# Performance work log

Measured on AMD Instinct MI355X. Metric: run time of the kernel, lower is better.

The kernel has to match this reference:

```python
import jax, jax.numpy as jnp
import numpy as np

DEPTH = 4
HEADS = 8
DIM_HEAD = 32
NUM_CLUSTERS = 64
KMEANS_ITERS = 10
EPS = 1e-5


def layer_norm(x, g, b):
    m = jnp.mean(x, axis=-1, keepdims=True)
    v = jnp.var(x, axis=-1, keepdims=True)
    return (x - m) * jax.lax.rsqrt(v + EPS) * g + b


def kmeans_cluster(xf, k, iters):
    # xf: [P, D]. Lloyd's algorithm with deterministic init (first k points).
    centers = xf[:k]
    x_sq = jnp.sum(xf * xf, axis=-1, keepdims=True)  # [P,1]

    def assign(c):
        # squared distances [P, K]
        d = x_sq - 2.0 * (xf @ c.T) + jnp.sum(c * c, axis=-1)[None, :]
        return jnp.argmin(d, axis=-1)

    def step(c, _):
        labels = assign(c)
        sums = jax.ops.segment_sum(xf, labels, num_segments=k)
        counts = jax.ops.segment_sum(jnp.ones((xf.shape[0],), xf.dtype), labels, num_segments=k)
        new_c = jnp.where(counts[:, None] > 0, sums / jnp.maximum(counts, 1.0)[:, None], c)
        return new_c, None

    centers, _ = jax.lax.scan(step, centers, None, length=iters)
    labels = assign(centers)
    return centers[labels]  # gather: [P, D]


def setup_inputs() -> dict:
    key = jax.random.key(0)
    ks = jax.random.split(key, 8)
    B, N, D, L, M = 8, 1024, 256, DEPTH, 1024
    s = 0.02
    return {
        "x": jax.random.normal(ks[0], (B, N, D), jnp.float32),
        "ln1_g": jnp.ones((L, D), jnp.float32),
        "ln1_b": jnp.zeros((L, D), jnp.float32),
        "Wq": jax.random.normal(ks[1], (L, D, HEADS * DIM_HEAD), jnp.float32) * s,
        "Wkv": jax.random.normal(ks[2], (L, D, 2 * HEADS * DIM_HEAD), jnp.float32) * s,
        "Wo": jax.random.normal(ks[3], (L, HEADS * DIM_HEAD, D), jnp.float32) * s,
        "bo": jnp.zeros((L, D), jnp.float32),
        "ln2_g": jnp.ones((L, D), jnp.float32),
        "ln2_b": jnp.zeros((L, D), jnp.float32),
        "W1": jax.random.normal(ks[4], (L, D, M), jnp.float32) * s,
        "b1": jnp.zeros((L, M), jnp.float32),
        "W2": jax.random.normal(ks[5], (L, M, D), jnp.float32) * s,
        "b2": jnp.zeros((L, D), jnp.float32),
        "kW": jax.random.normal(ks[6], (D, D), jnp.float32) * s,
        "kb": jnp.zeros((D,), jnp.float32),
    }


def reference(x, ln1_g, ln1_b, Wq, Wkv, Wo, bo, ln2_g, ln2_b, W1, b1, W2, b2, kW, kb):
    B, N, D = x.shape
    h, dh = HEADS, DIM_HEAD
    scale = dh ** -0.5
    for l in range(DEPTH):
        # PreNorm self-attention + residual
        xn = layer_norm(x, ln1_g[l], ln1_b[l])
        q = (xn @ Wq[l]).reshape(B, N, h, dh)
        kv = xn @ Wkv[l]
        k, v = jnp.split(kv, 2, axis=-1)
        k = k.reshape(B, N, h, dh)
        v = v.reshape(B, N, h, dh)
        dots = jnp.einsum("bqhd,bkhd->bhqk", q, k) * scale
        attn = jax.nn.softmax(dots, axis=-1)
        out = jnp.einsum("bhqk,bkhd->bqhd", attn, v).reshape(B, N, h * dh)
        x = out @ Wo[l] + bo[l] + x
        # PreNorm FFN + residual
        xn = layer_norm(x, ln2_g[l], ln2_b[l])
        hdd = jax.nn.gelu(xn @ W1[l] + b1[l], approximate=False)
        x = hdd @ W2[l] + b2[l] + x
    # KMeans module: cluster flattened tokens, gather centers, linear transform.
    xf = x.reshape(B * N, D)
    clustered = kmeans_cluster(xf, NUM_CLUSTERS, KMEANS_ITERS)
    clustered = jax.lax.stop_gradient(clustered)  # torch detaches before sklearn
    clustered = clustered.reshape(B, N, D)
    return clustered @ kW + kb
```

## Files before the change

kernel.cpp:

```cpp
#include <hip/hip_runtime.h>
#include <hip/hip_bf16.h>
#include <math.h>

#define BN 8192
#define DMODEL 256
#define FFN 1024
#define NCLUST 64

typedef unsigned short u16;
typedef unsigned int u32;
typedef __attribute__((ext_vector_type(8))) short s16x8;
typedef __attribute__((ext_vector_type(8))) unsigned short u16x8;
typedef __attribute__((ext_vector_type(4))) unsigned short u16x4;
typedef __attribute__((ext_vector_type(4))) float f32x4;

__device__ __forceinline__ float bf2f(u16 v) {
    union { unsigned int u; float f; } w; w.u = ((unsigned int)v) << 16; return w.f;
}
__device__ __forceinline__ u16 f2bf(float f) {
    union { float f; unsigned int u; } w; w.f = f;
    unsigned int r = w.u + 0x7fffu + ((w.u >> 16) & 1u);
    return (u16)(r >> 16);
}
__device__ __forceinline__ u32 cvtpk(float lo, float hi) {
    u32 r;
    asm("v_cvt_pk_bf16_f32 %0, %1, %2" : "=v"(r) : "v"(lo), "v"(hi));
    return r;
}
__device__ __forceinline__ float u2f(u32 u) { union { u32 u; float f; } w; w.u = u; return w.f; }

__device__ __forceinline__ void gl16(const u16* g, u16* l) {
    __builtin_amdgcn_global_load_lds((const __attribute__((address_space(1))) u32*)g,
                                     (__attribute__((address_space(3))) u32*)l, 16, 0, 0);
}

#define BARRIER_LGKM() asm volatile("s_waitcnt lgkmcnt(0)\n\ts_barrier" ::: "memory")
#define MEMFENCE_ORDER() asm volatile("" ::: "memory")

__device__ __forceinline__ int sw32(int row, int col) { return row * 32 + (col ^ (((row >> 1) & 3) << 3)); }
__device__ __forceinline__ int sw64(int row, int col) { return row * 64 + (col ^ ((row & 7) << 3)); }
template<int BK>
__device__ __forceinline__ int swk(int row, int col) {
    if constexpr (BK == 32) return row * 32 + (col ^ (((row >> 1) & 3) << 3));
    else                    return row * 64 + (col ^ ((row & 7) << 3));
}

__global__ __launch_bounds__(256) void ln_wave(const float* __restrict__ x, const float* __restrict__ g,
                                               const float* __restrict__ b, u16* __restrict__ yh,
                                               u16* __restrict__ yl) {
    int t = threadIdx.x, w = t >> 6, l = t & 63;
    int row = blockIdx.x * 4 + w;
    const float* xr = x + (size_t)row * DMODEL;
    float4 v = *reinterpret_cast<const float4*>(xr + l * 4);
    float s = v.x + v.y + v.z + v.w;
    for (int off = 1; off < 64; off <<= 1) s += __shfl_xor(s, off);
    float mean = s * (1.0f / 256.0f);
    float4 dv = make_float4(v.x - mean, v.y - mean, v.z - mean, v.w - mean);
    float vs = dv.x * dv.x + dv.y * dv.y + dv.z * dv.z + dv.w * dv.w;
    for (int off = 1; off < 64; off <<= 1) vs += __shfl_xor(vs, off);
    float rs = rsqrtf(vs * (1.0f / 256.0f) + 1e-5f);
    float4 gg = *reinterpret_cast<const float4*>(g + l * 4);
    float4 bb = *reinterpret_cast<const float4*>(b + l * 4);
    float os[4] = {dv.x * rs * gg.x + bb.x, dv.y * rs * gg.y + bb.y,
                   dv.z * rs * gg.z + bb.z, dv.w * rs * gg.w + bb.w};
    u16x4 hv, lv;
#pragma unroll
    for (int j = 0; j < 4; j++) { u16 hh = f2bf(os[j]); hv[j] = hh; lv[j] = f2bf(os[j] - bf2f(hh)); }
    size_t o = (size_t)row * DMODEL + l * 4;
    *reinterpret_cast<u16x4*>(yh + o) = hv;
    *reinterpret_cast<u16x4*>(yl + o) = lv;
}

__device__ __forceinline__ void wconv_body(const float* __restrict__ W, u16* __restrict__ th,
                                           u16* __restrict__ tl, int K, int N, int bx, int by) {
    __shared__ float T[64][65];
    int k0 = by * 64, n0 = bx * 64;
    int t = threadIdx.x;
    int r = t >> 4, c4 = (t & 15) * 4;
#pragma unroll
    for (int i = 0; i < 4; i++) {
        float4 x = *reinterpret_cast<const float4*>(W + (size_t)(k0 + r + 16 * i) * N + n0 + c4);
        T[r + 16 * i][c4] = x.x; T[r + 16 * i][c4 + 1] = x.y;
        T[r + 16 * i][c4 + 2] = x.z; T[r + 16 * i][c4 + 3] = x.w;
    }
    __syncthreads();
#pragma unroll
    for (int i = 0; i < 4; i++) {
        int n = r + 16 * i;
        u16x4 h4, l4;
#pragma unroll
        for (int j = 0; j < 4; j++) {
            float v = T[c4 + j][n];
            u16 h = f2bf(v);
            h4[j] = h; l4[j] = f2bf(v - bf2f(h));
        }
        *reinterpret_cast<u16x4*>(th + (size_t)(n0 + n) * K + k0 + c4) = h4;
        *reinterpret_cast<u16x4*>(tl + (size_t)(n0 + n) * K + k0 + c4) = l4;
    }
}

__global__ __launch_bounds__(256) void wconv_all(const float* __restrict__ Wq, const float* __restrict__ Wkv,
                                                 const float* __restrict__ Wo, const float* __restrict__ W1,
                                                 const float* __restrict__ W2,
                                                 u16* __restrict__ wqkvh, u16* __restrict__ wqkvl,
                                                 u16* __restrict__ woh, u16* __restrict__ wol,
                                                 u16* __restrict__ w1h, u16* __restrict__ w1l,
                                                 u16* __restrict__ w2h, u16* __restrict__ w2l) {
    int f = blockIdx.x;
    if (f < 16)       wconv_body(Wq,  wqkvh,               wqkvl,               256, 256,  f & 3,  f >> 2);
    else if (f < 48)  { int g = f - 16;  wconv_body(Wkv, wqkvh + 65536,       wqkvl + 65536,       256, 512,  g & 7,  g >> 3); }
    else if (f < 64)  { int g = f - 48;  wconv_body(Wo,  woh,                 wol,                 256, 256,  g & 3,  g >> 2); }
    else if (f < 128) { int g = f - 64;  wconv_body(W1,  w1h,                 w1l,                 256, 1024, g & 15, g >> 4); }
    else              { int g = f - 128; wconv_body(W2,  w2h,                 w2l,                 1024, 256, g & 3,  g >> 2); }
}

template<int BM, int BNT, int BK>
__global__ __launch_bounds__(256) void gemm_t(const u16* __restrict__ Ath, const u16* __restrict__ Atl,
                                              const u16* __restrict__ Bth, const u16* __restrict__ Btl,
                                              const float* __restrict__ bias, const float* __restrict__ resid,
                                              float* __restrict__ Cf, u16* __restrict__ Ch, u16* __restrict__ Cl,
                                              int M, int N, int K, int fuse_gelu) {
    __shared__ u16 Ah[2][BM * BK], Al[2][BM * BK];
    __shared__ u16 Bh[2][BNT * BK], Bl[2][BNT * BK];
    constexpr int WAVES_N = (BM == 128 && BNT == 64) ? 1 : 2;
    constexpr int WAVES_M = 4 / WAVES_N;
    constexpr int MI = BM / (16 * WAVES_M);
    constexpr int NI = BNT / (16 * WAVES_N);
    constexpr int SEGS = (BM + BNT) * BK / 1024;
    constexpr int ROWS_SEG = 512 / BK;
    constexpr int ASEG = BM / ROWS_SEG;
    constexpr int BSEG = BNT / ROWS_SEG;
    int t = threadIdx.x;
    int m0 = blockIdx.y * BM, n0 = blockIdx.x * BNT;
    int L = t & 63, w = t >> 6, fr = L & 15, quad = L >> 4;
    int wm = (WAVES_N == 1) ? w : (w & 1);
    int wn = (WAVES_N == 1) ? 0 : (w >> 1);

    const u16* gsrc[SEGS];
    u16* ldst[SEGS];
    u32 dlt[SEGS];
    {
        int lr, lc;
        if constexpr (BK == 32) { lr = L >> 2; lc = (L & 3) * 8; }
        else                    { lr = L >> 3; lc = (L & 7) * 8; }
#pragma unroll
        for (int i = 0; i < SEGS; i++) {
            int s = w * SEGS + i;
            const u16* gb; u16* lb; int r; u32 d;
            if (s < ASEG)                 { gb = Ath + (size_t)m0 * K; lb = &Ah[0][0]; r = s * ROWS_SEG;                 d = BM * BK; }
            else if (s < 2 * ASEG)        { gb = Atl + (size_t)m0 * K; lb = &Al[0][0]; r = (s - ASEG) * ROWS_SEG;        d = BM * BK; }
            else if (s < 2 * ASEG + BSEG) { gb = Bth + (size_t)n0 * K; lb = &Bh[0][0]; r = (s - 2 * ASEG) * ROWS_SEG;    d = BNT * BK; }
            else                          { gb = Btl + (size_t)n0 * K; lb = &Bl[0][0]; r = (s - 2 * ASEG - BSEG) * ROWS_SEG; d = BNT * BK; }
            int row = r + lr;
            int scol;
            if constexpr (BK == 32) scol = lc ^ (((row >> 1) & 3) << 3);
            else                    scol = lc ^ ((row & 7) << 3);
            gsrc[i] = gb + (size_t)row * K + scol;
            ldst[i] = lb + r * BK;
            dlt[i] = d;
        }
    }

    f32x4 acc[MI][NI];
#pragma unroll
    for (int i = 0; i < MI; i++)
#pragma unroll
        for (int j = 0; j < NI; j++) acc[i][j] = (f32x4){0.0f, 0.0f, 0.0f, 0.0f};

    const int NT = K / BK;
#pragma unroll
    for (int i = 0; i < SEGS; i++) gl16(gsrc[i], ldst[i]);

    for (int tt = 0; tt < NT; tt++) {
        asm volatile("s_waitcnt lgkmcnt(0)" ::: "memory");
        __builtin_amdgcn_s_barrier();
        if (tt + 1 < NT) {
            int k0n = (tt + 1) * BK;
            u32 sel = (u32)((tt + 1) & 1);
#pragma unroll
            for (int i = 0; i < SEGS; i++) gl16(gsrc[i] + k0n, ldst[i] + sel * dlt[i]);
            asm volatile("s_waitcnt vmcnt(%0)" :: "n"(SEGS) : "memory");
        } else {
            asm volatile("s_waitcnt vmcnt(0)" ::: "memory");
        }
        __builtin_amdgcn_s_barrier();
        __builtin_amdgcn_sched_barrier(0);
        int cb = tt & 1;
        const u16* AhB = &Ah[cb][0]; const u16* AlB = &Al[cb][0];
        const u16* BhB = &Bh[cb][0]; const u16* BlB = &Bl[cb][0];
#pragma unroll
        for (int kk = 0; kk < BK / 32; kk++) {
            int kc = kk * 32 + quad * 8;
            s16x8 ah[MI], al[MI];
#pragma unroll
            for (int mi = 0; mi < MI; mi++) {
                int row = wm * (MI * 16) + mi * 16 + fr;
                ah[mi] = *reinterpret_cast<const s16x8*>(&AhB[swk<BK>(row, kc)]);
                al[mi] = *reinterpret_cast<const s16x8*>(&AlB[swk<BK>(row, kc)]);
            }
            __builtin_amdgcn_s_setprio(1);
#pragma unroll
            for (int ni = 0; ni < NI; ni++) {
                int rn = wn * (NI * 16) + ni * 16 + fr;
                s16x8 bhf = *reinterpret_cast<const s16x8*>(&BhB[swk<BK>(rn, kc)]);
                s16x8 blf = *reinterpret_cast<const s16x8*>(&BlB[swk<BK>(rn, kc)]);
#pragma unroll
                for (int mi = 0; mi < MI; mi++) {
                    acc[mi][ni] = __builtin_amdgcn_mfma_f32_16x16x32_bf16(ah[mi], bhf, acc[mi][ni], 0, 0, 0);
                    acc[mi][ni] = __builtin_amdgcn_mfma_f32_16x16x32_bf16(ah[mi], blf, acc[mi][ni], 0, 0, 0);
                    acc[mi][ni] = __builtin_amdgcn_mfma_f32_16x16x32_bf16(al[mi], bhf, acc[mi][ni], 0, 0, 0);
                }
            }
            __builtin_amdgcn_s_setprio(0);
        }
    }
#pragma unroll
    for (int mi = 0; mi < MI; mi++) {
#pragma unroll
        for (int ni = 0; ni < NI; ni++) {
#pragma unroll
            for (int r = 0; r < 4; r++) {
                int row = m0 + wm * (MI * 16) + mi * 16 + quad * 4 + r;
                int col = n0 + wn * (NI * 16) + ni * 16 + fr;
                float v = acc[mi][ni][r];
                if (bias) v += bias[col];
                if (fuse_gelu) v = 0.5f * v * (1.0f + erff(v * 0.70710678118654752f));
                if (resid) v += resid[(size_t)row * N + col];
                size_t o = (size_t)row * N + col;
                if (Cf) Cf[o] = v;
                if (Ch) { u16 hh = f2bf(v); Ch[o] = hh; Cl[o] = f2bf(v - bf2f(hh)); }
            }
        }
    }
}

__global__ __launch_bounds__(256) void attn14(const u16* __restrict__ qkvh, const u16* __restrict__ qkvl,
                                              u16* __restrict__ aoh, u16* __restrict__ aol) {
    int bh = blockIdx.x, b = bh >> 3, h = bh & 7;
    int qt = blockIdx.y;
    int t = threadIdx.x, L = t & 63, w = t >> 6;
    int fr = L & 15, quad = L >> 4;
    __shared__ u16 KH[2][64 * 32], KL[2][64 * 32];
    __shared__ u16 VTH[32 * 64], VTL[32 * 64];
    __shared__ u16 PH[4][16 * 64], PL[4][16 * 64];
    const float scale = 0.17677669529663687f;
    const int ROWS = 768;

    const u16* ksrc[2];
    u16* kdst[2];
    {
        int lr = L >> 2, lc = (L & 3) * 8;
#pragma unroll
        for (int i = 0; i < 2; i++) {
            int s = w * 2 + i;
            const u16* gb = (s < 4) ? qkvh : qkvl;
            u16* lb = (s < 4) ? &KH[0][0] : &KL[0][0];
            int r = (s & 3) * 16;
            int row = r + lr;
            int scol = lc ^ (((row >> 1) & 3) << 3);
            ksrc[i] = gb + ((size_t)(b * 1024) + row) * ROWS + 256 + h * 32 + scol;
            kdst[i] = lb + r * 32;
        }
    }

    size_t qoff0 = (size_t)(b * 1024 + qt * 128 + w * 16 + fr) * ROWS + h * 32 + quad * 8;
    s16x8 aqh0 = *reinterpret_cast<const s16x8*>(qkvh + qoff0);
    s16x8 aql0 = *reinterpret_cast<const s16x8*>(qkvl + qoff0);
    s16x8 aqh1 = *reinterpret_cast<const s16x8*>(qkvh + qoff0 + (size_t)64 * ROWS);
    s16x8 aql1 = *reinterpret_cast<const s16x8*>(qkvl + qoff0 + (size_t)64 * ROWS);

    int vp = t >> 3, vd0 = (t & 7) * 4;
    const u16* vh_ptr = qkvh + (size_t)(b * 1024 + 2 * vp) * ROWS + 512 + h * 32 + vd0;
    const u16* vl_ptr = qkvl + (size_t)(b * 1024 + 2 * vp) * ROWS + 512 + h * 32 + vd0;
    u16x4 vh0, vh1, vl0, vl1;
#define LOADV(kt_) do { size_t o_ = (size_t)((kt_) * 64) * ROWS;                                  \
        vh0 = *reinterpret_cast<const u16x4*>(vh_ptr + o_);                                       \
        vh1 = *reinterpret_cast<const u16x4*>(vh_ptr + o_ + ROWS);                                \
        vl0 = *reinterpret_cast<const u16x4*>(vl_ptr + o_);                                       \
        vl1 = *reinterpret_cast<const u16x4*>(vl_ptr + o_ + ROWS); } while (0)

    gl16(ksrc[0], kdst[0]);
    gl16(ksrc[1], kdst[1]);
    MEMFENCE_ORDER();
    LOADV(0);

    float m_0 = -1e30f, l_0 = 0.0f, m_1 = -1e30f, l_1 = 0.0f;
    f32x4 accA0, accA1, accB0, accB1;
    accA0 = (f32x4){0.0f, 0.0f, 0.0f, 0.0f}; accA1 = accA0; accB0 = accA0; accB1 = accA0;

#define SM_PV(SV, M_I, L_I, ACC0, ACC1) do {                                                      \
        float p[16];                                                                              \
        float ml = -1e30f;                                                                        \
        _Pragma("unroll")                                                                         \
        for (int ni = 0; ni < 4; ni++)                                                            \
            _Pragma("unroll")                                                                     \
            for (int r = 0; r < 4; r++) { float v = SV[ni][r] * scale; p[ni * 4 + r] = v; ml = fmaxf(ml, v); } \
        ml = fmaxf(ml, __shfl_xor(ml, 16));                                                       \
        ml = fmaxf(ml, __shfl_xor(ml, 32));                                                       \
        float mnew = fmaxf(M_I, ml);                                                              \
        float alpha = __expf(M_I - mnew);                                                         \
        M_I = mnew;                                                                               \
        float rs = 0.0f;                                                                          \
        _Pragma("unroll")                                                                         \
        for (int i = 0; i < 16; i++) { float e = __expf(p[i] - mnew); p[i] = e; rs += e; }        \
        rs += __shfl_xor(rs, 16);                                                                 \
        rs += __shfl_xor(rs, 32);                                                                 \
        L_I = L_I * alpha + rs;                                                                   \
        _Pragma("unroll")                                                                         \
        for (int ni = 0; ni < 4; ni++) {                                                          \
            float p0 = p[ni * 4], p1 = p[ni * 4 + 1], p2 = p[ni * 4 + 2], p3 = p[ni * 4 + 3];     \
            u32 qh01 = cvtpk(p0, p1), qh23 = cvtpk(p2, p3);                                       \
            float e0 = p0 - u2f(qh01 << 16);                                                      \
            float e1 = p1 - u2f(qh01 & 0xffff0000u);                                              \
            float e2 = p2 - u2f(qh23 << 16);                                                      \
            float e3 = p3 - u2f(qh23 & 0xffff0000u);                                              \
            u32 ql01 = cvtpk(e0, e1), ql23 = cvtpk(e2, e3);                                       \
            int c0 = sw64(fr, ni * 16 + quad * 4);                                                \
            int c1 = sw64(fr, ni * 16 + quad * 4 + 2);                                            \
            *reinterpret_cast<u32*>(&PH[w][c0]) = qh01;                                           \
            *reinterpret_cast<u32*>(&PH[w][c1]) = qh23;                                           \
            *reinterpret_cast<u32*>(&PL[w][c0]) = ql01;                                           \
            *reinterpret_cast<u32*>(&PL[w][c1]) = ql23;                                           \
        }                                                                                         \
        float a4[4];                                                                              \
        _Pragma("unroll")                                                                         \
        for (int r = 0; r < 4; r++) a4[r] = __shfl(alpha, quad * 4 + r);                          \
        ACC0[0] *= a4[0]; ACC0[1] *= a4[1]; ACC0[2] *= a4[2]; ACC0[3] *= a4[3];                   \
        ACC1[0] *= a4[0]; ACC1[1] *= a4[1]; ACC1[2] *= a4[2]; ACC1[3] *= a4[3];                   \
        __builtin_amdgcn_s_setprio(1);                                                            \
        _Pragma("unroll")                                                                         \
        for (int ks = 0; ks < 2; ks++) {                                                          \
            s16x8 aph = *reinterpret_cast<s16x8*>(&PH[w][sw64(fr, ks * 32 + quad * 8)]);          \
            s16x8 apl = *reinterpret_cast<s16x8*>(&PL[w][sw64(fr, ks * 32 + quad * 8)]);          \
            s16x8 bvh0 = *reinterpret_cast<s16x8*>(&VTH[sw64(fr, ks * 32 + quad * 8)]);           \
            s16x8 bvl0 = *reinterpret_cast<s16x8*>(&VTL[sw64(fr, ks * 32 + quad * 8)]);           \
            ACC0 = __builtin_amdgcn_mfma_f32_16x16x32_bf16(aph, bvh0, ACC0, 0, 0, 0);             \
            ACC0 = __builtin_amdgcn_mfma_f32_16x16x32_bf16(aph, bvl0, ACC0, 0, 0, 0);             \
            ACC0 = __builtin_amdgcn_mfma_f32_16x16x32_bf16(apl, bvh0, ACC0, 0, 0, 0);             \
            s16x8 bvh1 = *reinterpret_cast<s16x8*>(&VTH[sw64(16 + fr, ks * 32 + quad * 8)]);      \
            s16x8 bvl1 = *reinterpret_cast<s16x8*>(&VTL[sw64(16 + fr, ks * 32 + quad * 8)]);      \
            ACC1 = __builtin_amdgcn_mfma_f32_16x16x32_bf16(aph, bvh1, ACC1, 0, 0, 0);             \
            ACC1 = __builtin_amdgcn_mfma_f32_16x16x32_bf16(aph, bvl1, ACC1, 0, 0, 0);             \
            ACC1 = __builtin_amdgcn_mfma_f32_16x16x32_bf16(apl, bvh1, ACC1, 0, 0, 0);             \
        }                                                                                         \
        __builtin_amdgcn_s_setprio(0);                                                            \
    } while (0)

#pragma unroll 2
    for (int kt = 0; kt < 16; kt++) {
        int cur = kt & 1;
        BARRIER_LGKM();
        if (kt < 15) {
            size_t koff = (size_t)((kt + 1) * 64) * ROWS;
            u32 sel = (u32)((kt + 1) & 1) * (64 * 32);
            gl16(ksrc[0] + koff, kdst[0] + sel);
            gl16(ksrc[1] + koff, kdst[1] + sel);
        }
        {
#pragma unroll
            for (int i = 0; i < 4; i++) {
                int idx = sw64(vd0 + i, 2 * vp);
                *reinterpret_cast<u32*>(&VTH[idx]) = (u32)vh0[i] | ((u32)vh1[i] << 16);
                *reinterpret_cast<u32*>(&VTL[idx]) = (u32)vl0[i] | ((u32)vl1[i] << 16);
            }
        }
        BARRIER_LGKM();
        f32x4 sv0[4], sv1[4];
        __builtin_amdgcn_s_setprio(1);
#pragma unroll
        for (int ni = 0; ni < 4; ni++) {
            s16x8 bkh = *reinterpret_cast<s16x8*>(&KH[cur][sw32(ni * 16 + fr, quad * 8)]);
            s16x8 bkl = *reinterpret_cast<s16x8*>(&KL[cur][sw32(ni * 16 + fr, quad * 8)]);
            f32x4 c0 = (f32x4){0.0f, 0.0f, 0.0f, 0.0f};
            c0 = __builtin_amdgcn_mfma_f32_16x16x32_bf16(bkh, aqh0, c0, 0, 0, 0);
            c0 = __builtin_amdgcn_mfma_f32_16x16x32_bf16(bkl, aqh0, c0, 0, 0, 0);
            c0 = __builtin_amdgcn_mfma_f32_16x16x32_bf16(bkh, aql0, c0, 0, 0, 0);
            sv0[ni] = c0;
            f32x4 c1 = (f32x4){0.0f, 0.0f, 0.0f, 0.0f};
            c1 = __builtin_amdgcn_mfma_f32_16x16x32_bf16(bkh, aqh1, c1, 0, 0, 0);
            c1 = __builtin_amdgcn_mfma_f32_16x16x32_bf16(bkl, aqh1, c1, 0, 0, 0);
            c1 = __builtin_amdgcn_mfma_f32_16x16x32_bf16(bkh, aql1, c1, 0, 0, 0);
            sv1[ni] = c1;
        }
        __builtin_amdgcn_s_setprio(0);
        if (kt < 15) LOADV(kt + 1);
        SM_PV(sv0, m_0, l_0, accA0, accA1);
        SM_PV(sv1, m_1, l_1, accB0, accB1);
    }
#undef SM_PV
#undef LOADV
    float invl0 = 1.0f / l_0, invl1 = 1.0f / l_1;
#pragma unroll
    for (int r = 0; r < 4; r++) {
        float iv0 = __shfl(invl0, quad * 4 + r);
        float iv1 = __shfl(invl1, quad * 4 + r);
        size_t rb0 = ((size_t)(b * 1024 + qt * 128 + w * 16 + quad * 4 + r)) * DMODEL + h * 32;
        size_t rb1 = rb0 + (size_t)64 * DMODEL;
        float v0 = accA0[r] * iv0, v1 = accA1[r] * iv0;
        u16 h0 = f2bf(v0); aoh[rb0 + fr] = h0;      aol[rb0 + fr] = f2bf(v0 - bf2f(h0));
        u16 h1 = f2bf(v1); aoh[rb0 + 16 + fr] = h1; aol[rb0 + 16 + fr] = f2bf(v1 - bf2f(h1));
        float v2 = accB0[r] * iv1, v3 = accB1[r] * iv1;
        u16 h2 = f2bf(v2); aoh[rb1 + fr] = h2;      aol[rb1 + fr] = f2bf(v2 - bf2f(h2));
        u16 h3 = f2bf(v3); aoh[rb1 + 16 + fr] = h3; aol[rb1 + 16 + fr] = f2bf(v3 - bf2f(h3));
    }
}

__global__ __launch_bounds__(64) void csq_k(const float* __restrict__ centers, float* __restrict__ csq) {
    int j = blockIdx.x, l = threadIdx.x;
    float4 c4 = *reinterpret_cast<const float4*>(centers + j * DMODEL + l * 4);
    float s = c4.x * c4.x + c4.y * c4.y + c4.z * c4.z + c4.w * c4.w;
    for (int off = 1; off < 64; off <<= 1) s += __shfl_xor(s, off);
    if (l == 0) csq[j] = s;
}

__global__ __launch_bounds__(256) void km_distmin(const float* __restrict__ A, const float* __restrict__ Cn,
                                                  const float* __restrict__ csq, int* __restrict__ labels) {
    __shared__ float As[16][34];
    __shared__ float Bs[16][64];
    int t = threadIdx.x, tx = t & 15, ty = t >> 4;
    int m0 = blockIdx.x * 32;
    int mr = t & 31, kq = (t >> 5) * 2;
    int jb = t & 63, kb = (t >> 6) * 4;
    float acc[2][4] = {};
    for (int k0 = 0; k0 < 256; k0 += 16) {
        __syncthreads();
        {
            float2 a2 = *reinterpret_cast<const float2*>(A + (size_t)(m0 + mr) * DMODEL + k0 + kq);
            As[kq][mr] = a2.x; As[kq + 1][mr] = a2.y;
        }
        {
            float4 c4 = *reinterpret_cast<const float4*>(Cn + (size_t)jb * DMODEL + k0 + kb);
            Bs[kb][jb] = c4.x; Bs[kb + 1][jb] = c4.y; Bs[kb + 2][jb] = c4.z; Bs[kb + 3][jb] = c4.w;
        }
        __syncthreads();
#pragma unroll
        for (int kk = 0; kk < 16; kk++) {
            float2 a2v = *reinterpret_cast<float2*>(&As[kk][ty * 2]);
            float4 b4 = *reinterpret_cast<float4*>(&Bs[kk][tx * 4]);
            float a[2] = {a2v.x, a2v.y};
            float bf[4] = {b4.x, b4.y, b4.z, b4.w};
#pragma unroll
            for (int i = 0; i < 2; i++)
#pragma unroll
                for (int j = 0; j < 4; j++) acc[i][j] += a[i] * bf[j];
        }
    }
    float4 cs4 = *reinterpret_cast<const float4*>(csq + tx * 4);
    float csv[4] = {cs4.x, cs4.y, cs4.z, cs4.w};
#pragma unroll
    for (int i = 0; i < 2; i++) {
        float best = csv[0] - 2.0f * acc[i][0]; int bi = tx * 4;
#pragma unroll
        for (int j = 1; j < 4; j++) {
            float v = csv[j] - 2.0f * acc[i][j];
            if (v < best) { best = v; bi = tx * 4 + j; }
        }
        for (int off = 1; off < 16; off <<= 1) {
            float ov = __shfl_xor(best, off);
            int oi = __shfl_xor(bi, off);
            if (ov < best || (ov == best && oi < bi)) { best = ov; bi = oi; }
        }
        if (tx == 0) labels[m0 + ty * 2 + i] = bi;
    }
}

__global__ __launch_bounds__(256) void km_segsum(const int* __restrict__ labels, const float* __restrict__ xf,
                                                 float* __restrict__ sums16, float* __restrict__ counts16) {
    int c = blockIdx.x, j = blockIdx.y, t = threadIdx.x;
    __shared__ int labs[512];
    if (t < 128) {
        int4 l4 = *reinterpret_cast<const int4*>(labels + c * 512 + t * 4);
        labs[t * 4] = l4.x; labs[t * 4 + 1] = l4.y; labs[t * 4 + 2] = l4.z; labs[t * 4 + 3] = l4.w;
    }
    __syncthreads();
    float acc = 0.0f, cnt = 0.0f;
    const float* xb = xf + (size_t)c * 512 * DMODEL;
    for (int i = 0; i < 512; i++) {
        if (labs[i] == j) { acc += xb[(size_t)i * DMODEL + t]; cnt += 1.0f; }
    }
    sums16[((size_t)c * NCLUST + j) * DMODEL + t] = acc;
    if (t == 0) counts16[c * NCLUST + j] = cnt;
}

__global__ __launch_bounds__(256) void km_update(float* __restrict__ centers, const float* __restrict__ sums16,
                                                 const float* __restrict__ counts16, float* __restrict__ csq) {
    __shared__ float red[256];
    int j = blockIdx.x, d = threadIdx.x;
    float c = 0.0f;
#pragma unroll
    for (int cc = 0; cc < 16; cc++) c += counts16[cc * NCLUST + j];
    float sv = 0.0f;
#pragma unroll
    for (int cc = 0; cc < 16; cc++) sv += sums16[((size_t)cc * NCLUST + j) * DMODEL + d];
    float cv = centers[j * DMODEL + d];
    if (c > 0.0f) cv = sv / fmaxf(c, 1.0f);
    centers[j * DMODEL + d] = cv;
    red[d] = cv * cv;
    __syncthreads();
    for (int off = 128; off; off >>= 1) { if (d < off) red[d] += red[d + off]; __syncthreads(); }
    if (d == 0) csq[j] = red[0];
}

__global__ __launch_bounds__(256) void nproj(const float* __restrict__ centers, const float* __restrict__ kW,
                                             const float* __restrict__ kb2, float* __restrict__ outc) {
    int idx = blockIdx.x * 256 + threadIdx.x;
    if (idx >= NCLUST * DMODEL) return;
    int row = idx >> 8, col = idx & 255;
    const float* cr = centers + row * DMODEL;
    float acc = 0.0f;
    for (int d = 0; d < DMODEL; d++) acc += cr[d] * kW[(size_t)d * DMODEL + col];
    outc[idx] = acc + kb2[col];
}

__global__ __launch_bounds__(256) void km_gather(const int* __restrict__ labels, const float* __restrict__ outc,
                                                 float* __restrict__ out) {
    int t = threadIdx.x;
#pragma unroll
    for (int r = 0; r < 4; r++) {
        int i = blockIdx.x * 4 + r;
        int lab = labels[i];
        out[(size_t)i * DMODEL + t] = outc[lab * DMODEL + t];
    }
}

extern "C" void kernel_launch(void* const* d_in, const int* in_sizes, int n_in,
                              void* d_out, int out_size, void* d_ws, size_t ws_size,
                              hipStream_t stream) {
    const float* x_in  = (const float*)d_in[0];
    const float* ln1_g = (const float*)d_in[1];
    const float* ln1_b = (const float*)d_in[2];
    const float* Wq    = (const float*)d_in[3];
    const float* Wkv   = (const float*)d_in[4];
    const float* Wo    = (const float*)d_in[5];
    const float* bo    = (const float*)d_in[6];
    const float* ln2_g = (const float*)d_in[7];
    const float* ln2_b = (const float*)d_in[8];
    const float* W1    = (const float*)d_in[9];
    const float* b1    = (const float*)d_in[10];
    const float* W2    = (const float*)d_in[11];
    const float* b2    = (const float*)d_in[12];
    const float* kWp   = (const float*)d_in[13];
    const float* kbp   = (const float*)d_in[14];
    float* out = (float*)d_out;

    const size_t NEEDED = 53477376;
    if (ws_size < NEEDED) {
        hipMemsetAsync(d_out, 0, (size_t)out_size * sizeof(float), stream);
        return;
    }

    char* ws = (char*)d_ws;
    float* xf      = (float*)(ws);
    u16*   xnh     = (u16*)  (ws + 8388608);
    u16*   xnl     = (u16*)  (ws + 12582912);
    u16*   aoh     = xnh;
    u16*   aol     = xnl;
    u16*   qkvh    = (u16*)  (ws + 16777216);
    u16*   qkvl    = (u16*)  (ws + 29360128);
    u16*   hbh     = (u16*)  (ws + 16777216);
    u16*   hbl     = (u16*)  (ws + 33554432);
    float* centers = (float*)(ws + 41943040);
    float* csqb    = (float*)(ws + 42008576);
    float* counts16= (float*)(ws + 42008832);
    int*   labels  = (int*)  (ws + 42012928);
    float* outc    = (float*)(ws + 42045696);
    float* sums16  = (float*)(ws + 42111232);
    u16*   wr      = (u16*)  (ws + 50331648);
    u16 *wqkvh = wr,          *wqkvl = wr + 196608;
    u16 *woh = wr + 393216,   *wol = wr + 458752;
    u16 *w1h = wr + 524288,   *w1l = wr + 786432;
    u16 *w2h = wr + 1048576,  *w2l = wr + 1310720;

    hipMemcpyAsync(xf, x_in, (size_t)BN * DMODEL * sizeof(float), hipMemcpyDeviceToDevice, stream);

    for (int l = 0; l < 4; l++) {
        wconv_all<<<192, 256, 0, stream>>>(Wq + (size_t)l * 65536, Wkv + (size_t)l * 131072,
                                           Wo + (size_t)l * 65536, W1 + (size_t)l * 262144,
                                           W2 + (size_t)l * 262144,
                                           wqkvh, wqkvl, woh, wol, w1h, w1l, w2h, w2l);

        ln_wave<<<BN / 4, 256, 0, stream>>>(xf, ln1_g + l * 256, ln1_b + l * 256, xnh, xnl);
        gemm_t<128, 128, 32><<<dim3(6, 64), 256, 0, stream>>>(xnh, xnl, wqkvh, wqkvl, nullptr, nullptr,
                                                              nullptr, qkvh, qkvl, BN, 768, 256, 0);
        attn14<<<dim3(64, 8), 256, 0, stream>>>(qkvh, qkvl, aoh, aol);
        gemm_t<64, 64, 64><<<dim3(4, 128), 256, 0, stream>>>(aoh, aol, woh, wol, bo + l * 256, xf,
                                                             xf, nullptr, nullptr, BN, 256, 256, 0);
        ln_wave<<<BN / 4, 256, 0, stream>>>(xf, ln2_g + l * 256, ln2_b + l * 256, xnh, xnl);
        gemm_t<128, 128, 32><<<dim3(8, 64), 256, 0, stream>>>(xnh, xnl, w1h, w1l, b1 + l * 1024, nullptr,
                                                              nullptr, hbh, hbl, BN, 1024, 256, 1);
        gemm_t<64, 64, 64><<<dim3(4, 128), 256, 0, stream>>>(hbh, hbl, w2h, w2l, b2 + l * 256, xf,
                                                             xf, nullptr, nullptr, BN, 256, 1024, 0);
    }

    hipMemcpyAsync(centers, xf, NCLUST * DMODEL * sizeof(float), hipMemcpyDeviceToDevice, stream);
    csq_k<<<64, 64, 0, stream>>>(centers, csqb);
    for (int it = 0; it < 10; it++) {
        km_distmin<<<256, 256, 0, stream>>>(xf, centers, csqb, labels);
        km_segsum<<<dim3(16, NCLUST), 256, 0, stream>>>(labels, xf, sums16, counts16);
        km_update<<<64, 256, 0, stream>>>(centers, sums16, counts16, csqb);
    }
    km_distmin<<<256, 256, 0, stream>>>(xf, centers, csqb, labels);
    nproj<<<64, 256, 0, stream>>>(centers, kWp, kbp, outc);
    km_gather<<<BN / 4, 256, 0, stream>>>(labels, outc, out);
}
```

Before: 1.263 ms.

## Batch attention PV MFMAs across both query subtiles, use exp2, retile kmeans distmin

```diff
diff --git a/kernel.cpp b/kernel.cpp
--- a/kernel.cpp
+++ b/kernel.cpp
@@ -234,7 +234,7 @@
     }
 }
 
-__global__ __launch_bounds__(256) void attn14(const u16* __restrict__ qkvh, const u16* __restrict__ qkvl,
+__global__ __launch_bounds__(256) void attn15(const u16* __restrict__ qkvh, const u16* __restrict__ qkvl,
                                               u16* __restrict__ aoh, u16* __restrict__ aol) {
     int bh = blockIdx.x, b = bh >> 3, h = bh & 7;
     int qt = blockIdx.y;
@@ -242,8 +242,8 @@
     int fr = L & 15, quad = L >> 4;
     __shared__ u16 KH[2][64 * 32], KL[2][64 * 32];
     __shared__ u16 VTH[32 * 64], VTL[32 * 64];
-    __shared__ u16 PH[4][16 * 64], PL[4][16 * 64];
-    const float scale = 0.17677669529663687f;
+    __shared__ u16 PH[2][4][16 * 64], PL[2][4][16 * 64];
+    const float scl2 = 0.17677669529663687f * 1.4426950408889634f;
     const int ROWS = 768;
 
     const u16* ksrc[2];
@@ -288,21 +288,21 @@
     f32x4 accA0, accA1, accB0, accB1;
     accA0 = (f32x4){0.0f, 0.0f, 0.0f, 0.0f}; accA1 = accA0; accB0 = accA0; accB1 = accA0;
 
-#define SM_PV(SV, M_I, L_I, ACC0, ACC1) do {                                                      \
+#define SM(SV, M_I, L_I, ACC0, ACC1, SUB) do {                                                    \
         float p[16];                                                                              \
         float ml = -1e30f;                                                                        \
         _Pragma("unroll")                                                                         \
         for (int ni = 0; ni < 4; ni++)                                                            \
             _Pragma("unroll")                                                                     \
-            for (int r = 0; r < 4; r++) { float v = SV[ni][r] * scale; p[ni * 4 + r] = v; ml = fmaxf(ml, v); } \
+            for (int r = 0; r < 4; r++) { float v = SV[ni][r] * scl2; p[ni * 4 + r] = v; ml = fmaxf(ml, v); } \
         ml = fmaxf(ml, __shfl_xor(ml, 16));                                                       \
         ml = fmaxf(ml, __shfl_xor(ml, 32));                                                       \
         float mnew = fmaxf(M_I, ml);                                                              \
-        float alpha = __expf(M_I - mnew);                                                         \
+        float alpha = exp2f(M_I - mnew);                                                          \
         M_I = mnew;                                                                               \
         float rs = 0.0f;                                                                          \
         _Pragma("unroll")                                                                         \
-        for (int i = 0; i < 16; i++) { float e = __expf(p[i] - mnew); p[i] = e; rs += e; }        \
+        for (int i = 0; i < 16; i++) { float e = exp2f(p[i] - mnew); p[i] = e; rs += e; }         \
         rs += __shfl_xor(rs, 16);                                                                 \
         rs += __shfl_xor(rs, 32);                                                                 \
         L_I = L_I * alpha + rs;                                                                   \
@@ -317,33 +317,16 @@
             u32 ql01 = cvtpk(e0, e1), ql23 = cvtpk(e2, e3);                                       \
             int c0 = sw64(fr, ni * 16 + quad * 4);                                                \
             int c1 = sw64(fr, ni * 16 + quad * 4 + 2);                                            \
-            *reinterpret_cast<u32*>(&PH[w][c0]) = qh01;                                           \
-            *reinterpret_cast<u32*>(&PH[w][c1]) = qh23;                                           \
-            *reinterpret_cast<u32*>(&PL[w][c0]) = ql01;                                           \
-            *reinterpret_cast<u32*>(&PL[w][c1]) = ql23;                                           \
+            *reinterpret_cast<u32*>(&PH[SUB][w][c0]) = qh01;                                      \
+            *reinterpret_cast<u32*>(&PH[SUB][w][c1]) = qh23;                                      \
+            *reinterpret_cast<u32*>(&PL[SUB][w][c0]) = ql01;                                      \
+            *reinterpret_cast<u32*>(&PL[SUB][w][c1]) = ql23;                                      \
         }                                                                                         \
         float a4[4];                                                                              \
         _Pragma("unroll")                                                                         \
         for (int r = 0; r < 4; r++) a4[r] = __shfl(alpha, quad * 4 + r);                          \
         ACC0[0] *= a4[0]; ACC0[1] *= a4[1]; ACC0[2] *= a4[2]; ACC0[3] *= a4[3];                   \
         ACC1[0] *= a4[0]; ACC1[1] *= a4[1]; ACC1[2] *= a4[2]; ACC1[3] *= a4[3];                   \
-        __builtin_amdgcn_s_setprio(1);                                                            \
-        _Pragma("unroll")                                                                         \
-        for (int ks = 0; ks < 2; ks++) {                                                          \
-            s16x8 aph = *reinterpret_cast<s16x8*>(&PH[w][sw64(fr, ks * 32 + quad * 8)]);          \
-            s16x8 apl = *reinterpret_cast<s16x8*>(&PL[w][sw64(fr, ks * 32 + quad * 8)]);          \
-            s16x8 bvh0 = *reinterpret_cast<s16x8*>(&VTH[sw64(fr, ks * 32 + quad * 8)]);           \
-            s16x8 bvl0 = *reinterpret_cast<s16x8*>(&VTL[sw64(fr, ks * 32 + quad * 8)]);           \
-            ACC0 = __builtin_amdgcn_mfma_f32_16x16x32_bf16(aph, bvh0, ACC0, 0, 0, 0);             \
-            ACC0 = __builtin_amdgcn_mfma_f32_16x16x32_bf16(aph, bvl0, ACC0, 0, 0, 0);             \
-            ACC0 = __builtin_amdgcn_mfma_f32_16x16x32_bf16(apl, bvh0, ACC0, 0, 0, 0);             \
-            s16x8 bvh1 = *reinterpret_cast<s16x8*>(&VTH[sw64(16 + fr, ks * 32 + quad * 8)]);      \
-            s16x8 bvl1 = *reinterpret_cast<s16x8*>(&VTL[sw64(16 + fr, ks * 32 + quad * 8)]);      \
-            ACC1 = __builtin_amdgcn_mfma_f32_16x16x32_bf16(aph, bvh1, ACC1, 0, 0, 0);             \
-            ACC1 = __builtin_amdgcn_mfma_f32_16x16x32_bf16(aph, bvl1, ACC1, 0, 0, 0);             \
-            ACC1 = __builtin_amdgcn_mfma_f32_16x16x32_bf16(apl, bvh1, ACC1, 0, 0, 0);             \
-        }                                                                                         \
-        __builtin_amdgcn_s_setprio(0);                                                            \
     } while (0)
 
 #pragma unroll 2
@@ -384,10 +367,40 @@
         }
         __builtin_amdgcn_s_setprio(0);
         if (kt < 15) LOADV(kt + 1);
-        SM_PV(sv0, m_0, l_0, accA0, accA1);
-        SM_PV(sv1, m_1, l_1, accB0, accB1);
-    }
-#undef SM_PV
+        SM(sv0, m_0, l_0, accA0, accA1, 0);
+        SM(sv1, m_1, l_1, accB0, accB1, 1);
+        __builtin_amdgcn_s_setprio(1);
+#pragma unroll
+        for (int ks = 0; ks < 2; ks++) {
+            int pc = sw64(fr, ks * 32 + quad * 8);
+            s16x8 aph0 = *reinterpret_cast<s16x8*>(&PH[0][w][pc]);
+            s16x8 apl0 = *reinterpret_cast<s16x8*>(&PL[0][w][pc]);
+            s16x8 aph1 = *reinterpret_cast<s16x8*>(&PH[1][w][pc]);
+            s16x8 apl1 = *reinterpret_cast<s16x8*>(&PL[1][w][pc]);
+            {
+                s16x8 bvh = *reinterpret_cast<s16x8*>(&VTH[sw64(fr, ks * 32 + quad * 8)]);
+                s16x8 bvl = *reinterpret_cast<s16x8*>(&VTL[sw64(fr, ks * 32 + quad * 8)]);
+                accA0 = __builtin_amdgcn_mfma_f32_16x16x32_bf16(aph0, bvh, accA0, 0, 0, 0);
+                accA0 = __builtin_amdgcn_mfma_f32_16x16x32_bf16(aph0, bvl, accA0, 0, 0, 0);
+                accA0 = __builtin_amdgcn_mfma_f32_16x16x32_bf16(apl0, bvh, accA0, 0, 0, 0);
+                accB0 = __builtin_amdgcn_mfma_f32_16x16x32_bf16(aph1, bvh, accB0, 0, 0, 0);
+                accB0 = __builtin_amdgcn_mfma_f32_16x16x32_bf16(aph1, bvl, accB0, 0, 0, 0);
+                accB0 = __builtin_amdgcn_mfma_f32_16x16x32_bf16(apl1, bvh, accB0, 0, 0, 0);
+            }
+            {
+                s16x8 bvh = *reinterpret_cast<s16x8*>(&VTH[sw64(16 + fr, ks * 32 + quad * 8)]);
+                s16x8 bvl = *reinterpret_cast<s16x8*>(&VTL[sw64(16 + fr, ks * 32 + quad * 8)]);
+                accA1 = __builtin_amdgcn_mfma_f32_16x16x32_bf16(aph0, bvh, accA1, 0, 0, 0);
+                accA1 = __builtin_amdgcn_mfma_f32_16x16x32_bf16(aph0, bvl, accA1, 0, 0, 0);
+                accA1 = __builtin_amdgcn_mfma_f32_16x16x32_bf16(apl0, bvh, accA1, 0, 0, 0);
+                accB1 = __builtin_amdgcn_mfma_f32_16x16x32_bf16(aph1, bvh, accB1, 0, 0, 0);
+                accB1 = __builtin_amdgcn_mfma_f32_16x16x32_bf16(aph1, bvl, accB1, 0, 0, 0);
+                accB1 = __builtin_amdgcn_mfma_f32_16x16x32_bf16(apl1, bvh, accB1, 0, 0, 0);
+            }
+        }
+        __builtin_amdgcn_s_setprio(0);
+    }
+#undef SM
 #undef LOADV
     float invl0 = 1.0f / l_0, invl1 = 1.0f / l_1;
 #pragma unroll
@@ -415,19 +428,16 @@
 
 __global__ __launch_bounds__(256) void km_distmin(const float* __restrict__ A, const float* __restrict__ Cn,
                                                   const float* __restrict__ csq, int* __restrict__ labels) {
-    __shared__ float As[16][34];
+    __shared__ float As[16][17];
     __shared__ float Bs[16][64];
     int t = threadIdx.x, tx = t & 15, ty = t >> 4;
-    int m0 = blockIdx.x * 32;
-    int mr = t & 31, kq = (t >> 5) * 2;
+    int m0 = blockIdx.x * 16;
+    int mr = t >> 4, kq = t & 15;
     int jb = t & 63, kb = (t >> 6) * 4;
-    float acc[2][4] = {};
+    float acc[4] = {};
     for (int k0 = 0; k0 < 256; k0 += 16) {
         __syncthreads();
-        {
-            float2 a2 = *reinterpret_cast<const float2*>(A + (size_t)(m0 + mr) * DMODEL + k0 + kq);
-            As[kq][mr] = a2.x; As[kq + 1][mr] = a2.y;
-        }
+        As[kq][mr] = A[(size_t)(m0 + mr) * DMODEL + k0 + kq];
         {
             float4 c4 = *reinterpret_cast<const float4*>(Cn + (size_t)jb * DMODEL + k0 + kb);
             Bs[kb][jb] = c4.x; Bs[kb + 1][jb] = c4.y; Bs[kb + 2][jb] = c4.z; Bs[kb + 3][jb] = c4.w;
@@ -435,33 +445,25 @@
         __syncthreads();
 #pragma unroll
         for (int kk = 0; kk < 16; kk++) {
-            float2 a2v = *reinterpret_cast<float2*>(&As[kk][ty * 2]);
+            float a = As[kk][ty];
             float4 b4 = *reinterpret_cast<float4*>(&Bs[kk][tx * 4]);
-            float a[2] = {a2v.x, a2v.y};
-            float bf[4] = {b4.x, b4.y, b4.z, b4.w};
-#pragma unroll
-            for (int i = 0; i < 2; i++)
-#pragma unroll
-                for (int j = 0; j < 4; j++) acc[i][j] += a[i] * bf[j];
+            acc[0] += a * b4.x; acc[1] += a * b4.y; acc[2] += a * b4.z; acc[3] += a * b4.w;
         }
     }
     float4 cs4 = *reinterpret_cast<const float4*>(csq + tx * 4);
     float csv[4] = {cs4.x, cs4.y, cs4.z, cs4.w};
-#pragma unroll
-    for (int i = 0; i < 2; i++) {
-        float best = csv[0] - 2.0f * acc[i][0]; int bi = tx * 4;
-#pragma unroll
-        for (int j = 1; j < 4; j++) {
-            float v = csv[j] - 2.0f * acc[i][j];
-            if (v < best) { best = v; bi = tx * 4 + j; }
-        }
-        for (int off = 1; off < 16; off <<= 1) {
-            float ov = __shfl_xor(best, off);
-            int oi = __shfl_xor(bi, off);
-            if (ov < best || (ov == best && oi < bi)) { best = ov; bi = oi; }
-        }
-        if (tx == 0) labels[m0 + ty * 2 + i] = bi;
-    }
+    float best = csv[0] - 2.0f * acc[0]; int bi = tx * 4;
+#pragma unroll
+    for (int j = 1; j < 4; j++) {
+        float v = csv[j] - 2.0f * acc[j];
+        if (v < best) { best = v; bi = tx * 4 + j; }
+    }
+    for (int off = 1; off < 16; off <<= 1) {
+        float ov = __shfl_xor(best, off);
+        int oi = __shfl_xor(bi, off);
+        if (ov < best || (ov == best && oi < bi)) { best = ov; bi = oi; }
+    }
+    if (tx == 0) labels[m0 + ty] = bi;
 }
 
 __global__ __launch_bounds__(256) void km_segsum(const int* __restrict__ labels, const float* __restrict__ xf,
@@ -582,7 +584,7 @@
         ln_wave<<<BN / 4, 256, 0, stream>>>(xf, ln1_g + l * 256, ln1_b + l * 256, xnh, xnl);
         gemm_t<128, 128, 32><<<dim3(6, 64), 256, 0, stream>>>(xnh, xnl, wqkvh, wqkvl, nullptr, nullptr,
                                                               nullptr, qkvh, qkvl, BN, 768, 256, 0);
-        attn14<<<dim3(64, 8), 256, 0, stream>>>(qkvh, qkvl, aoh, aol);
+        attn15<<<dim3(64, 8), 256, 0, stream>>>(qkvh, qkvl, aoh, aol);
         gemm_t<64, 64, 64><<<dim3(4, 128), 256, 0, stream>>>(aoh, aol, woh, wol, bo + l * 256, xf,
                                                              xf, nullptr, nullptr, BN, 256, 256, 0);
         ln_wave<<<BN / 4, 256, 0, stream>>>(xf, ln2_g + l * 256, ln2_b + l * 256, xnh, xnl);
@@ -595,11 +597,11 @@
     hipMemcpyAsync(centers, xf, NCLUST * DMODEL * sizeof(float), hipMemcpyDeviceToDevice, stream);
     csq_k<<<64, 64, 0, stream>>>(centers, csqb);
     for (int it = 0; it < 10; it++) {
-        km_distmin<<<256, 256, 0, stream>>>(xf, centers, csqb, labels);
+        km_distmin<<<512, 256, 0, stream>>>(xf, centers, csqb, labels);
         km_segsum<<<dim3(16, NCLUST), 256, 0, stream>>>(labels, xf, sums16, counts16);
         km_update<<<64, 256, 0, stream>>>(centers, sums16, counts16, csqb);
     }
-    km_distmin<<<256, 256, 0, stream>>>(xf, centers, csqb, labels);
+    km_distmin<<<512, 256, 0, stream>>>(xf, centers, csqb, labels);
     nproj<<<64, 256, 0, stream>>>(centers, kWp, kbp, outc);
     km_gather<<<BN / 4, 256, 0, stream>>>(labels, outc, out);
 }
```

Result: slower. 1.318 ms (+4.4%).
